# Kernel tuning notes

Hardware: AMD Instinct MI355X
Metric: run time of the kernel (lower is better)

Reference implementation:

```python
import jax, jax.numpy as jnp
import numpy as np

NUM_HEADS = 16
THETA = 10000.0

def _rope(t, token_ids, theta):
    # t: [B, H, S, Dk]; token_ids: [S]
    d_k = t.shape[-1]
    inv_freq = theta ** (-jnp.arange(0, d_k, 2, dtype=jnp.float32) / d_k)  # [Dk/2]
    ang = token_ids.astype(jnp.float32)[:, None] * inv_freq[None, :]       # [S, Dk/2]
    cos, sin = jnp.cos(ang), jnp.sin(ang)
    x1, x2 = t[..., ::2], t[..., 1::2]
    r1 = x1 * cos - x2 * sin
    r2 = x1 * sin + x2 * cos
    return jnp.stack([r1, r2], axis=-1).reshape(t.shape)

def setup_inputs() -> dict:
    key = jax.random.key(0)
    ks = jax.random.split(key, 5)
    d_model = 1024
    scale = 0.02
    return {
        "x": jax.random.normal(ks[0], (4, 2048, d_model), dtype=jnp.float32),
        "token_ids": jnp.arange(2048, dtype=jnp.int32),
        "Wq": jax.random.normal(ks[1], (d_model, d_model), dtype=jnp.float32) * scale,
        "Wk": jax.random.normal(ks[2], (d_model, d_model), dtype=jnp.float32) * scale,
        "Wv": jax.random.normal(ks[3], (d_model, d_model), dtype=jnp.float32) * scale,
        "Wo": jax.random.normal(ks[4], (d_model, d_model), dtype=jnp.float32) * scale,
    }

def reference(x, token_ids, Wq, Wk, Wv, Wo):
    B, S, D = x.shape
    H = NUM_HEADS
    Dk = D // H
    def split_heads(t):
        return t.reshape(B, S, H, Dk).transpose(0, 2, 1, 3)  # [B,H,S,Dk]
    q = split_heads(x @ Wq.T)
    k = split_heads(x @ Wk.T)
    v = split_heads(x @ Wv.T)
    q = _rope(q, token_ids, THETA)
    k = _rope(k, token_ids, THETA)
    scores = jnp.einsum("bhqd,bhkd->bhqk", q, k) / jnp.sqrt(jnp.float32(Dk))
    causal = jnp.tril(jnp.ones((S, S), dtype=bool))
    scores = jnp.where(causal, scores, jnp.float32(-1e9))
    attn = jax.nn.softmax(scores, axis=-1)
    out = jnp.einsum("bhqk,bhkd->bhqd", attn, v)
    out = out.transpose(0, 2, 1, 3).reshape(B, S, H * Dk)
    return out @ Wo.T
```

## Files before the change

### kernel.cpp

```cpp
#include <hip/hip_runtime.h>

#define BATCH 4
#define SLEN 2048
#define DMODEL 1024
#define NHEADS 16
#define DK 64
#define MROWS (BATCH * SLEN)
#define NQB 16
#define SCALE_LOG2E 0.1803368801111731f

typedef short bf16x8 __attribute__((ext_vector_type(8)));
typedef unsigned short u16x4 __attribute__((ext_vector_type(4)));
typedef float f32x4 __attribute__((ext_vector_type(4)));

__device__ __forceinline__ unsigned short f2bf(float f) {
    unsigned u = __float_as_uint(f);
    unsigned r = u + 0x7FFFu + ((u >> 16) & 1u);
    return (unsigned short)(r >> 16);
}

__device__ __forceinline__ unsigned pkbf(float a, float b) {
    unsigned r;
    asm volatile("v_cvt_pk_bf16_f32 %0, %1, %2" : "=v"(r) : "v"(a), "v"(b));
    return r;
}

__device__ __forceinline__ void gload_lds16(const void* g, void* l) {
    __builtin_amdgcn_global_load_lds(
        (const __attribute__((address_space(1))) void*)g,
        (__attribute__((address_space(3))) void*)l, 16, 0, 0);
}

__global__ void cvt_f32_bf16(const float* __restrict__ in, unsigned short* __restrict__ out, int n) {
    int i = (blockIdx.x * blockDim.x + threadIdx.x) * 4;
    if (i >= n) return;
    float4 v = *reinterpret_cast<const float4*>(in + i);
    u16x4 o;
    o[0] = f2bf(v.x); o[1] = f2bf(v.y); o[2] = f2bf(v.z); o[3] = f2bf(v.w);
    *reinterpret_cast<u16x4*>(out + i) = o;
}

__global__ void cvt_w_all(const float* __restrict__ w0, const float* __restrict__ w1,
                          const float* __restrict__ w2, const float* __restrict__ w3,
                          unsigned short* __restrict__ o0, unsigned short* __restrict__ o1,
                          unsigned short* __restrict__ o2, unsigned short* __restrict__ o3) {
    int z = blockIdx.y;
    const float* src = (z == 0) ? w0 : (z == 1) ? w1 : (z == 2) ? w2 : w3;
    unsigned short* dst = (z == 0) ? o0 : (z == 1) ? o1 : (z == 2) ? o2 : o3;
    int i = (blockIdx.x * blockDim.x + threadIdx.x) * 4;
    float4 v = *reinterpret_cast<const float4*>(src + i);
    u16x4 o;
    o[0] = f2bf(v.x); o[1] = f2bf(v.y); o[2] = f2bf(v.z); o[3] = f2bf(v.w);
    *reinterpret_cast<u16x4*>(dst + i) = o;
}

__global__ void rope_table(const int* __restrict__ tok, float* __restrict__ cs, float* __restrict__ sn) {
    int idx = blockIdx.x * blockDim.x + threadIdx.x;
    if (idx >= SLEN * 32) return;
    int s = idx >> 5, fi = idx & 31;
    float invf = powf(10000.0f, -(float)(2 * fi) / 64.0f);
    float ang = (float)tok[s] * invf;
    cs[idx] = cosf(ang);
    sn[idx] = sinf(ang);
}

__device__ __forceinline__ void gemm128_core(
    const unsigned short* __restrict__ A, const unsigned short* __restrict__ B,
    int m0, int n0, int tid, f32x4 (&acc)[4][4],
    unsigned short* As, unsigned short* Bs)
{
    int lane = tid & 63, wave = tid >> 6;
    int ln = lane & 15, kq = lane >> 4;
    int wr = wave >> 1, wc = wave & 1;
#pragma unroll
    for (int a = 0; a < 4; a++)
#pragma unroll
        for (int b = 0; b < 4; b++) acc[a][b] = (f32x4){0.f, 0.f, 0.f, 0.f};

    for (int k0 = 0; k0 < DMODEL; k0 += 64) {
        if (k0) __syncthreads();
#pragma unroll
        for (int i = 0; i < 4; i++) {
            int s = i * 256 + tid;
            int r = s >> 3;
            int u = (s & 7) ^ (r & 7);
            gload_lds16(A + (size_t)(m0 + r) * DMODEL + k0 + u * 8, &As[(i * 256 + wave * 64) * 8]);
            gload_lds16(B + (size_t)(n0 + r) * DMODEL + k0 + u * 8, &Bs[(i * 256 + wave * 64) * 8]);
        }
        __syncthreads();

        bf16x8 af[4][2], bfr[4][2];
#pragma unroll
        for (int mt = 0; mt < 4; mt++) {
            int row = wr * 64 + mt * 16 + ln;
#pragma unroll
            for (int kc = 0; kc < 2; kc++) {
                int u = (kc * 4 + kq) ^ (row & 7);
                af[mt][kc] = *reinterpret_cast<const bf16x8*>(&As[row * 64 + u * 8]);
            }
        }
#pragma unroll
        for (int nt = 0; nt < 4; nt++) {
            int row = wc * 64 + nt * 16 + ln;
#pragma unroll
            for (int kc = 0; kc < 2; kc++) {
                int u = (kc * 4 + kq) ^ (row & 7);
                bfr[nt][kc] = *reinterpret_cast<const bf16x8*>(&Bs[row * 64 + u * 8]);
            }
        }
        __builtin_amdgcn_s_setprio(1);
#pragma unroll
        for (int kc = 0; kc < 2; kc++)
#pragma unroll
            for (int mt = 0; mt < 4; mt++)
#pragma unroll
                for (int nt = 0; nt < 4; nt++)
                    acc[mt][nt] = __builtin_amdgcn_mfma_f32_16x16x32_bf16(af[mt][kc], bfr[nt][kc], acc[mt][nt], 0, 0, 0);
        __builtin_amdgcn_s_setprio(0);
    }
}

__global__ __launch_bounds__(256) void qkv_gemm(
    const unsigned short* __restrict__ X,
    const unsigned short* __restrict__ Wq,
    const unsigned short* __restrict__ Wk,
    const unsigned short* __restrict__ Wv,
    const float* __restrict__ cs_tab, const float* __restrict__ sn_tab,
    unsigned short* __restrict__ Q, unsigned short* __restrict__ K,
    unsigned short* __restrict__ VT)
{
    __shared__ alignas(16) unsigned short As[128 * 64];
    __shared__ alignas(16) unsigned short Bs[128 * 64];
    int tid = threadIdx.x, lane = tid & 63, wave = tid >> 6;
    int ln = lane & 15, kq = lane >> 4;
    int wr = wave >> 1, wc = wave & 1;
    int m0 = blockIdx.x * 128;
    int n0 = blockIdx.y * 128;
    int z = blockIdx.z;
    const unsigned short* W = (z == 0) ? Wq : (z == 1) ? Wk : Wv;

    f32x4 acc[4][4];
    gemm128_core(X, W, m0, n0, tid, acc, As, Bs);

    bool isV = (z == 2);
    bool isQ = (z == 0);
    unsigned short* dstQK = (z == 0) ? Q : K;
    int m0w = m0 + wr * 64, n0w = n0 + wc * 64;
#pragma unroll
    for (int nt = 0; nt < 4; nt++) {
        int n = n0w + nt * 16 + ln;
        int h = n >> 6, d = n & 63;
        int fi = d >> 1;
#pragma unroll
        for (int mt = 0; mt < 4; mt++) {
#pragma unroll
            for (int j = 0; j < 4; j++) {
                int m = m0w + mt * 16 + kq * 4 + j;
                int b = m >> 11, s = m & (SLEN - 1);
                float v = acc[mt][nt][j];
                if (!isV) {
                    float c = cs_tab[s * 32 + fi];
                    float si = sn_tab[s * 32 + fi];
                    float p = __shfl_xor(v, 1);
                    v = (d & 1) ? (p * si + v * c) : (v * c - p * si);
                    if (isQ) v *= SCALE_LOG2E;
                    dstQK[(((size_t)(b * NHEADS + h) * SLEN + s) << 6) + d] = f2bf(v);
                } else {
                    VT[((size_t)(b * NHEADS + h) * DK + d) * SLEN + s] = f2bf(v);
                }
            }
        }
    }
}

__global__ __launch_bounds__(256, 4) void attn_kernel(
    const unsigned short* __restrict__ Q, const unsigned short* __restrict__ K,
    const unsigned short* __restrict__ VT, unsigned short* __restrict__ O)
{
    __shared__ alignas(16) unsigned short Kt[2][4096];
    __shared__ alignas(16) unsigned short Vt[2][4096];

    int tid = threadIdx.x, lane = tid & 63, wave = tid >> 6;
    int ln = lane & 15, kq = lane >> 4;
    int qb = blockIdx.x;
    int h = blockIdx.y, b = blockIdx.z;
    size_t headoff = ((size_t)b * NHEADS + h) * SLEN * DK;
    const unsigned short* Qh = Q + headoff;
    const unsigned short* Kh = K + headoff;
    const unsigned short* Vh = VT + headoff;

    auto stage = [&](int buf, int t) {
        int kv0 = t << 6;
#pragma unroll
        for (int i = 0; i < 2; i++) {
            int s = i * 256 + tid;
            int r = s >> 3;
            int cb = (s & 7) ^ (r & 7);
            int rp = ((r >> 5) << 5) | (((r >> 2) & 3) << 3) | (((r >> 4) & 1) << 2) | (r & 3);
            gload_lds16(Kh + (size_t)(kv0 + rp) * DK + cb * 8,
                        &Kt[buf][(i * 256 + wave * 64) * 8]);
            gload_lds16(Vh + (size_t)r * SLEN + kv0 + cb * 8,
                        &Vt[buf][(i * 256 + wave * 64) * 8]);
        }
    };

    for (int sid = 0; sid < 2; sid++) {
        int qs = sid ? qb : (NQB - 1 - qb);
        int q0 = qs * 128 + wave * 32;

        bf16x8 aq[2][2];
#pragma unroll
        for (int mt = 0; mt < 2; mt++)
#pragma unroll
            for (int kc = 0; kc < 2; kc++)
                aq[mt][kc] = *reinterpret_cast<const bf16x8*>(
                    Qh + (size_t)(q0 + mt * 16 + ln) * DK + kc * 32 + kq * 8);

        f32x4 oacc[2][4];
#pragma unroll
        for (int mt = 0; mt < 2; mt++)
#pragma unroll
            for (int nt = 0; nt < 4; nt++) oacc[mt][nt] = (f32x4){0.f, 0.f, 0.f, 0.f};
        float m_r[2] = {-1e30f, -1e30f};
        float l_r[2] = {0.f, 0.f};

        int tmax_w = (q0 + 31) >> 6;
        int ntiles = 2 * qs + 2;

        stage(0, 0);
        __syncthreads();

        for (int t = 0; t < ntiles; t++) {
            int buf = t & 1;
            if (t + 1 < ntiles) stage(buf ^ 1, t + 1);

            if (t <= tmax_w) {
                int kv0 = t << 6;
                f32x4 sacc[2][4];
#pragma unroll
                for (int mt = 0; mt < 2; mt++)
#pragma unroll
                    for (int nt = 0; nt < 4; nt++) sacc[mt][nt] = (f32x4){0.f, 0.f, 0.f, 0.f};
                __builtin_amdgcn_s_setprio(1);
#pragma unroll
                for (int nt = 0; nt < 4; nt++) {
                    int rr = nt * 16 + ln;
#pragma unroll
                    for (int kc = 0; kc < 2; kc++) {
                        int unit = (kc * 4 + kq) ^ (rr & 7);
                        bf16x8 bk = *reinterpret_cast<const bf16x8*>(&Kt[buf][rr * 64 + unit * 8]);
#pragma unroll
                        for (int mt = 0; mt < 2; mt++)
                            sacc[mt][nt] = __builtin_amdgcn_mfma_f32_16x16x32_bf16(bk, aq[mt][kc], sacc[mt][nt], 0, 0, 0);
                    }
                }
                __builtin_amdgcn_s_setprio(0);

                if (kv0 + 63 > q0) {
#pragma unroll
                    for (int mt = 0; mt < 2; mt++) {
                        int q = q0 + mt * 16 + ln;
#pragma unroll
                        for (int nt = 0; nt < 4; nt++)
#pragma unroll
                            for (int j = 0; j < 4; j++) {
                                int k = kv0 + (nt >> 1) * 32 + kq * 8 + (nt & 1) * 4 + j;
                                if (k > q) sacc[mt][nt][j] = -1e30f;
                            }
                    }
                }

                float mloc[2];
#pragma unroll
                for (int mt = 0; mt < 2; mt++) {
                    f32x4 m4 = sacc[mt][0];
#pragma unroll
                    for (int nt = 1; nt < 4; nt++) {
                        m4[0] = fmaxf(m4[0], sacc[mt][nt][0]);
                        m4[1] = fmaxf(m4[1], sacc[mt][nt][1]);
                        m4[2] = fmaxf(m4[2], sacc[mt][nt][2]);
                        m4[3] = fmaxf(m4[3], sacc[mt][nt][3]);
                    }
                    mloc[mt] = fmaxf(fmaxf(m4[0], m4[1]), fmaxf(m4[2], m4[3]));
                }
#pragma unroll
                for (int mt = 0; mt < 2; mt++) {
                    mloc[mt] = fmaxf(mloc[mt], __shfl_xor(mloc[mt], 16));
                    mloc[mt] = fmaxf(mloc[mt], __shfl_xor(mloc[mt], 32));
                }

                bool needscale = !__all((mloc[0] <= m_r[0] + 8.0f) && (mloc[1] <= m_r[1] + 8.0f));
                float so[2] = {1.f, 1.f};
                if (needscale) {
#pragma unroll
                    for (int mt = 0; mt < 2; mt++) {
                        float mn = fmaxf(m_r[mt], mloc[mt]);
                        so[mt] = exp2f(m_r[mt] - mn);
                        m_r[mt] = mn;
                    }
                }

                float rs[2] = {0.f, 0.f};
#pragma unroll
                for (int mt = 0; mt < 2; mt++)
#pragma unroll
                    for (int nt = 0; nt < 4; nt++)
#pragma unroll
                        for (int j = 0; j < 4; j++) {
                            float p = exp2f(sacc[mt][nt][j] - m_r[mt]);
                            sacc[mt][nt][j] = p;
                            rs[mt] += p;
                        }
#pragma unroll
                for (int mt = 0; mt < 2; mt++) {
                    rs[mt] += __shfl_xor(rs[mt], 16);
                    rs[mt] += __shfl_xor(rs[mt], 32);
                    l_r[mt] = l_r[mt] * so[mt] + rs[mt];
                }

                if (needscale) {
                    float so_o[2][4];
#pragma unroll
                    for (int mt = 0; mt < 2; mt++)
#pragma unroll
                        for (int j = 0; j < 4; j++)
                            so_o[mt][j] = __shfl(so[mt], kq * 4 + j, 16);
#pragma unroll
                    for (int mt = 0; mt < 2; mt++)
#pragma unroll
                        for (int nt = 0; nt < 4; nt++)
#pragma unroll
                            for (int j = 0; j < 4; j++)
                                oacc[mt][nt][j] *= so_o[mt][j];
                }

                bf16x8 pa[2][2];
#pragma unroll
                for (int mt = 0; mt < 2; mt++)
#pragma unroll
                    for (int kc = 0; kc < 2; kc++) {
                        union { unsigned u[4]; bf16x8 v; } r;
                        r.u[0] = pkbf(sacc[mt][2 * kc][0], sacc[mt][2 * kc][1]);
                        r.u[1] = pkbf(sacc[mt][2 * kc][2], sacc[mt][2 * kc][3]);
                        r.u[2] = pkbf(sacc[mt][2 * kc + 1][0], sacc[mt][2 * kc + 1][1]);
                        r.u[3] = pkbf(sacc[mt][2 * kc + 1][2], sacc[mt][2 * kc + 1][3]);
                        pa[mt][kc] = r.v;
                    }

                __builtin_amdgcn_s_setprio(1);
#pragma unroll
                for (int nt = 0; nt < 4; nt++) {
                    int rr = nt * 16 + ln;
#pragma unroll
                    for (int kc = 0; kc < 2; kc++) {
                        int unit = (kc * 4 + kq) ^ (rr & 7);
                        bf16x8 bv = *reinterpret_cast<const bf16x8*>(&Vt[buf][rr * 64 + unit * 8]);
#pragma unroll
                        for (int mt = 0; mt < 2; mt++)
                            oacc[mt][nt] = __builtin_amdgcn_mfma_f32_16x16x32_bf16(pa[mt][kc], bv, oacc[mt][nt], 0, 0, 0);
                    }
                }
                __builtin_amdgcn_s_setprio(0);
            }
            __syncthreads();
        }

        float lo[2][4];
#pragma unroll
        for (int mt = 0; mt < 2; mt++)
#pragma unroll
            for (int j = 0; j < 4; j++)
                lo[mt][j] = __shfl(l_r[mt], kq * 4 + j, 16);
#pragma unroll
        for (int mt = 0; mt < 2; mt++)
#pragma unroll
            for (int nt = 0; nt < 4; nt++)
#pragma unroll
                for (int j = 0; j < 4; j++) {
                    int row = q0 + mt * 16 + kq * 4 + j;
                    float v = oacc[mt][nt][j] / lo[mt][j];
                    O[((size_t)b * SLEN + row) * DMODEL + h * 64 + nt * 16 + ln] = f2bf(v);
                }
        __syncthreads();
    }
}

__global__ __launch_bounds__(256) void out_gemm(
    const unsigned short* __restrict__ A, const unsigned short* __restrict__ Wo,
    float* __restrict__ out)
{
    __shared__ alignas(16) unsigned short As[128 * 64];
    __shared__ alignas(16) unsigned short Bs[128 * 64];
    int tid = threadIdx.x, lane = tid & 63, wave = tid >> 6;
    int ln = lane & 15, kq = lane >> 4;
    int wr = wave >> 1, wc = wave & 1;
    int m0 = blockIdx.x * 128;
    int n0 = blockIdx.y * 128;

    f32x4 acc[4][4];
    gemm128_core(A, Wo, m0, n0, tid, acc, As, Bs);

    int m0w = m0 + wr * 64, n0w = n0 + wc * 64;
#pragma unroll
    for (int mt = 0; mt < 4; mt++)
#pragma unroll
        for (int nt = 0; nt < 4; nt++)
#pragma unroll
            for (int j = 0; j < 4; j++) {
                int m = m0w + mt * 16 + kq * 4 + j;
                int n = n0w + nt * 16 + ln;
                out[(size_t)m * DMODEL + n] = acc[mt][nt][j];
            }
}

extern "C" void kernel_launch(void* const* d_in, const int* in_sizes, int n_in,
                              void* d_out, int out_size, void* d_ws, size_t ws_size,
                              hipStream_t stream) {
    const float* x  = (const float*)d_in[0];
    const int* tok  = (const int*)d_in[1];
    const float* wq = (const float*)d_in[2];
    const float* wk = (const float*)d_in[3];
    const float* wv = (const float*)d_in[4];
    const float* wo = (const float*)d_in[5];
    float* out = (float*)d_out;

    const size_t XB_OFF = 0;
    const size_t WQ_OFF = 16777216;
    const size_t WK_OFF = 18874368;
    const size_t WV_OFF = 20971520;
    const size_t WO_OFF = 23068672;
    const size_t Q_OFF  = 25165824;
    const size_t K_OFF  = 41943040;
    const size_t VT_OFF = 58720256;
    const size_t O_OFF  = 75497472;
    const size_t CS_OFF = 92274688;
    const size_t SN_OFF = 92536832;
    const size_t WS_NEEDED = 92798976;
    if (ws_size < WS_NEEDED) return;

    char* ws = (char*)d_ws;
    unsigned short* Xb  = (unsigned short*)(ws + XB_OFF);
    unsigned short* Wqb = (unsigned short*)(ws + WQ_OFF);
    unsigned short* Wkb = (unsigned short*)(ws + WK_OFF);
    unsigned short* Wvb = (unsigned short*)(ws + WV_OFF);
    unsigned short* Wob = (unsigned short*)(ws + WO_OFF);
    unsigned short* Qb  = (unsigned short*)(ws + Q_OFF);
    unsigned short* Kb  = (unsigned short*)(ws + K_OFF);
    unsigned short* VTb = (unsigned short*)(ws + VT_OFF);
    unsigned short* Ob  = (unsigned short*)(ws + O_OFF);
    float* cs_tab = (float*)(ws + CS_OFF);
    float* sn_tab = (float*)(ws + SN_OFF);

    cvt_f32_bf16<<<8192, 256, 0, stream>>>(x, Xb, MROWS * DMODEL);
    cvt_w_all<<<dim3(1024, 4), 256, 0, stream>>>(wq, wk, wv, wo, Wqb, Wkb, Wvb, Wob);
    rope_table<<<256, 256, 0, stream>>>(tok, cs_tab, sn_tab);

    qkv_gemm<<<dim3(MROWS / 128, DMODEL / 128, 3), 256, 0, stream>>>(
        Xb, Wqb, Wkb, Wvb, cs_tab, sn_tab, Qb, Kb, VTb);

    attn_kernel<<<dim3(SLEN / 256, NHEADS, BATCH), 256, 0, stream>>>(Qb, Kb, VTb, Ob);

    out_gemm<<<dim3(MROWS / 128, DMODEL / 128, 1), 256, 0, stream>>>(Ob, Wob, out);
}
```

Measured before the change: 214.6 us.

## Rewrite QKV GEMM with 256x256 tiles and multi-buffered async LDS pipeline

Result: slower. 661.7 us (+208.4%).

```diff
diff --git a/kernel.cpp b/kernel.cpp
--- a/kernel.cpp
+++ b/kernel.cpp
@@ -64,63 +64,7 @@
     sn[idx] = sinf(ang);
 }
 
-__device__ __forceinline__ void gemm128_core(
-    const unsigned short* __restrict__ A, const unsigned short* __restrict__ B,
-    int m0, int n0, int tid, f32x4 (&acc)[4][4],
-    unsigned short* As, unsigned short* Bs)
-{
-    int lane = tid & 63, wave = tid >> 6;
-    int ln = lane & 15, kq = lane >> 4;
-    int wr = wave >> 1, wc = wave & 1;
-#pragma unroll
-    for (int a = 0; a < 4; a++)
-#pragma unroll
-        for (int b = 0; b < 4; b++) acc[a][b] = (f32x4){0.f, 0.f, 0.f, 0.f};
-
-    for (int k0 = 0; k0 < DMODEL; k0 += 64) {
-        if (k0) __syncthreads();
-#pragma unroll
-        for (int i = 0; i < 4; i++) {
-            int s = i * 256 + tid;
-            int r = s >> 3;
-            int u = (s & 7) ^ (r & 7);
-            gload_lds16(A + (size_t)(m0 + r) * DMODEL + k0 + u * 8, &As[(i * 256 + wave * 64) * 8]);
-            gload_lds16(B + (size_t)(n0 + r) * DMODEL + k0 + u * 8, &Bs[(i * 256 + wave * 64) * 8]);
-        }
-        __syncthreads();
-
-        bf16x8 af[4][2], bfr[4][2];
-#pragma unroll
-        for (int mt = 0; mt < 4; mt++) {
-            int row = wr * 64 + mt * 16 + ln;
-#pragma unroll
-            for (int kc = 0; kc < 2; kc++) {
-                int u = (kc * 4 + kq) ^ (row & 7);
-                af[mt][kc] = *reinterpret_cast<const bf16x8*>(&As[row * 64 + u * 8]);
-            }
-        }
-#pragma unroll
-        for (int nt = 0; nt < 4; nt++) {
-            int row = wc * 64 + nt * 16 + ln;
-#pragma unroll
-            for (int kc = 0; kc < 2; kc++) {
-                int u = (kc * 4 + kq) ^ (row & 7);
-                bfr[nt][kc] = *reinterpret_cast<const bf16x8*>(&Bs[row * 64 + u * 8]);
-            }
-        }
-        __builtin_amdgcn_s_setprio(1);
-#pragma unroll
-        for (int kc = 0; kc < 2; kc++)
-#pragma unroll
-            for (int mt = 0; mt < 4; mt++)
-#pragma unroll
-                for (int nt = 0; nt < 4; nt++)
-                    acc[mt][nt] = __builtin_amdgcn_mfma_f32_16x16x32_bf16(af[mt][kc], bfr[nt][kc], acc[mt][nt], 0, 0, 0);
-        __builtin_amdgcn_s_setprio(0);
-    }
-}
-
-__global__ __launch_bounds__(256) void qkv_gemm(
+__global__ __launch_bounds__(512, 4) void qkv_gemm(
     const unsigned short* __restrict__ X,
     const unsigned short* __restrict__ Wq,
     const unsigned short* __restrict__ Wk,
@@ -129,30 +73,99 @@
     unsigned short* __restrict__ Q, unsigned short* __restrict__ K,
     unsigned short* __restrict__ VT)
 {
-    __shared__ alignas(16) unsigned short As[128 * 64];
-    __shared__ alignas(16) unsigned short Bs[128 * 64];
-    int tid = threadIdx.x, lane = tid & 63, wave = tid >> 6;
-    int ln = lane & 15, kq = lane >> 4;
-    int wr = wave >> 1, wc = wave & 1;
-    int m0 = blockIdx.x * 128;
-    int n0 = blockIdx.y * 128;
-    int z = blockIdx.z;
+    __shared__ alignas(16) unsigned short Al[3][256 * 32];
+    __shared__ alignas(16) unsigned short Bl[2][256 * 32];
+    const int tid = threadIdx.x, lane = tid & 63, wave = tid >> 6;
+    const int ln = lane & 15, kq = lane >> 4;
+    const int wr = wave >> 2, wc = wave & 3;
+    const int m0 = blockIdx.x * 256;
+    const int n0 = blockIdx.y * 256;
+    const int z = blockIdx.z;
     const unsigned short* W = (z == 0) ? Wq : (z == 1) ? Wk : Wv;
 
-    f32x4 acc[4][4];
-    gemm128_core(X, W, m0, n0, tid, acc, As, Bs);
+    auto stA = [&](int buf, int kt) {
+#pragma unroll
+        for (int l = 0; l < 2; l++) {
+            int s = l * 512 + tid;
+            int r = s >> 2;
+            int cb = (s & 3) ^ ((r >> 1) & 3);
+            gload_lds16(X + (size_t)(m0 + r) * DMODEL + kt * 32 + cb * 8,
+                        &Al[buf][(l * 512 + wave * 64) * 8]);
+        }
+    };
+    auto stB = [&](int buf, int kt) {
+#pragma unroll
+        for (int l = 0; l < 2; l++) {
+            int s = l * 512 + tid;
+            int r = s >> 2;
+            int cb = (s & 3) ^ ((r >> 1) & 3);
+            gload_lds16(W + (size_t)(n0 + r) * DMODEL + kt * 32 + cb * 8,
+                        &Bl[buf][(l * 512 + wave * 64) * 8]);
+        }
+    };
+
+    f32x4 acc[8][4];
+#pragma unroll
+    for (int a = 0; a < 8; a++)
+#pragma unroll
+        for (int b = 0; b < 4; b++) acc[a][b] = (f32x4){0.f, 0.f, 0.f, 0.f};
+
+    stA(0, 0); stB(0, 0); stA(1, 1);
+    asm volatile("s_waitcnt vmcnt(2)" ::: "memory");
+    __builtin_amdgcn_s_barrier();
+    __builtin_amdgcn_sched_barrier(0);
+
+    const int NK = DMODEL / 32;
+    int abuf = 0;
+    for (int kt = 0; kt < NK; ++kt) {
+        const int bbuf = kt & 1;
+        if (kt + 2 < NK) { int a2 = abuf + 2; if (a2 >= 3) a2 -= 3; stA(a2, kt + 2); }
+        if (kt + 1 < NK) { stB(bbuf ^ 1, kt + 1); }
+        if (kt + 2 < NK)      { asm volatile("s_waitcnt vmcnt(4)" ::: "memory"); }
+        else if (kt + 1 < NK) { asm volatile("s_waitcnt vmcnt(2)" ::: "memory"); }
+        else                  { asm volatile("s_waitcnt vmcnt(0)" ::: "memory"); }
+        __builtin_amdgcn_s_barrier();
+        __builtin_amdgcn_sched_barrier(0);
+
+        bf16x8 af[8], bq[4];
+#pragma unroll
+        for (int mt = 0; mt < 8; mt++) {
+            int row = wr * 128 + mt * 16 + ln;
+            int u = kq ^ ((row >> 1) & 3);
+            af[mt] = *reinterpret_cast<const bf16x8*>(&Al[abuf][(row * 4 + u) * 8]);
+        }
+#pragma unroll
+        for (int nt = 0; nt < 4; nt++) {
+            int row = wc * 64 + nt * 16 + ln;
+            int u = kq ^ ((row >> 1) & 3);
+            bq[nt] = *reinterpret_cast<const bf16x8*>(&Bl[bbuf][(row * 4 + u) * 8]);
+        }
+        asm volatile("s_waitcnt lgkmcnt(0)" ::: "memory");
+        __builtin_amdgcn_sched_barrier(0);
+        __builtin_amdgcn_s_barrier();
+
+        __builtin_amdgcn_s_setprio(1);
+#pragma unroll
+        for (int mt = 0; mt < 8; mt++)
+#pragma unroll
+            for (int nt = 0; nt < 4; nt++)
+                acc[mt][nt] = __builtin_amdgcn_mfma_f32_16x16x32_bf16(af[mt], bq[nt], acc[mt][nt], 0, 0, 0);
+        __builtin_amdgcn_s_setprio(0);
+
+        abuf++; if (abuf == 3) abuf = 0;
+    }
 
     bool isV = (z == 2);
     bool isQ = (z == 0);
     unsigned short* dstQK = (z == 0) ? Q : K;
-    int m0w = m0 + wr * 64, n0w = n0 + wc * 64;
+    int m0w = m0 + wr * 128, n0w = n0 + wc * 64;
 #pragma unroll
     for (int nt = 0; nt < 4; nt++) {
         int n = n0w + nt * 16 + ln;
         int h = n >> 6, d = n & 63;
         int fi = d >> 1;
 #pragma unroll
-        for (int mt = 0; mt < 4; mt++) {
+        for (int mt = 0; mt < 8; mt++) {
 #pragma unroll
             for (int j = 0; j < 4; j++) {
                 int m = m0w + mt * 16 + kq * 4 + j;
@@ -173,6 +186,62 @@
     }
 }
 
+__device__ __forceinline__ void gemm128_core_sb(
+    const unsigned short* __restrict__ A, const unsigned short* __restrict__ B,
+    int m0, int n0, int tid, f32x4 (&acc)[4][4],
+    unsigned short* As, unsigned short* Bs)
+{
+    int lane = tid & 63, wave = tid >> 6;
+    int ln = lane & 15, kq = lane >> 4;
+    int wr = wave >> 1, wc = wave & 1;
+#pragma unroll
+    for (int a = 0; a < 4; a++)
+#pragma unroll
+        for (int b = 0; b < 4; b++) acc[a][b] = (f32x4){0.f, 0.f, 0.f, 0.f};
+
+    for (int k0 = 0; k0 < DMODEL; k0 += 64) {
+        if (k0) __syncthreads();
+#pragma unroll
+        for (int i = 0; i < 4; i++) {
+            int s = i * 256 + tid;
+            int r = s >> 3;
+            int u = (s & 7) ^ (r & 7);
+            gload_lds16(A + (size_t)(m0 + r) * DMODEL + k0 + u * 8, &As[(i * 256 + wave * 64) * 8]);
+            gload_lds16(B + (size_t)(n0 + r) * DMODEL + k0 + u * 8, &Bs[(i * 256 + wave * 64) * 8]);
+        }
+        __syncthreads();
+
+        bf16x8 af[4][2], bfr[4][2];
+#pragma unroll
+        for (int mt = 0; mt < 4; mt++) {
+            int row = wr * 64 + mt * 16 + ln;
+#pragma unroll
+            for (int kc = 0; kc < 2; kc++) {
+                int u = (kc * 4 + kq) ^ (row & 7);
+                af[mt][kc] = *reinterpret_cast<const bf16x8*>(&As[row * 64 + u * 8]);
+            }
+        }
+#pragma unroll
+        for (int nt = 0; nt < 4; nt++) {
+            int row = wc * 64 + nt * 16 + ln;
+#pragma unroll
+            for (int kc = 0; kc < 2; kc++) {
+                int u = (kc * 4 + kq) ^ (row & 7);
+                bfr[nt][kc] = *reinterpret_cast<const bf16x8*>(&Bs[row * 64 + u * 8]);
+            }
+        }
+        __builtin_amdgcn_s_setprio(1);
+#pragma unroll
+        for (int kc = 0; kc < 2; kc++)
+#pragma unroll
+            for (int mt = 0; mt < 4; mt++)
+#pragma unroll
+                for (int nt = 0; nt < 4; nt++)
+                    acc[mt][nt] = __builtin_amdgcn_mfma_f32_16x16x32_bf16(af[mt][kc], bfr[nt][kc], acc[mt][nt], 0, 0, 0);
+        __builtin_amdgcn_s_setprio(0);
+    }
+}
+
 __global__ __launch_bounds__(256, 4) void attn_kernel(
     const unsigned short* __restrict__ Q, const unsigned short* __restrict__ K,
     const unsigned short* __restrict__ VT, unsigned short* __restrict__ O)
@@ -398,7 +467,7 @@
     int n0 = blockIdx.y * 128;
 
     f32x4 acc[4][4];
-    gemm128_core(A, Wo, m0, n0, tid, acc, As, Bs);
+    gemm128_core_sb(A, Wo, m0, n0, tid, acc, As, Bs);
 
     int m0w = m0 + wr * 64, n0w = n0 + wc * 64;
 #pragma unroll
@@ -455,7 +524,7 @@
     cvt_w_all<<<dim3(1024, 4), 256, 0, stream>>>(wq, wk, wv, wo, Wqb, Wkb, Wvb, Wob);
     rope_table<<<256, 256, 0, stream>>>(tok, cs_tab, sn_tab);
 
-    qkv_gemm<<<dim3(MROWS / 128, DMODEL / 128, 3), 256, 0, stream>>>(
+    qkv_gemm<<<dim3(MROWS / 256, DMODEL / 256, 3), 512, 0, stream>>>(
         Xb, Wqb, Wkb, Wvb, cs_tab, sn_tab, Qb, Kb, VTb);
 
     attn_kernel<<<dim3(SLEN / 256, NHEADS, BATCH), 256, 0, stream>>>(Qb, Kb, VTb, Ob);
```
